# Performance work log

Measured on AMD Instinct MI355X. Metric: run time of the kernel, lower is better.

The kernel has to match this reference:

```python
import jax, jax.numpy as jnp
import numpy as np

DIM = 1024


def setup_inputs() -> dict:
    key = jax.random.key(0)
    ks = jax.random.split(key, 10)
    B, S, D = 4, 2048, DIM
    std = 1.0 / np.sqrt(D)  # torch Linear default uniform bound
    return {
        "query": jax.random.normal(ks[0], (B, S, D), jnp.float32),
        "key": jax.random.normal(ks[1], (B, S, D), jnp.float32),
        "value": jax.random.normal(ks[2], (B, S, D), jnp.float32),
        "context": jnp.zeros((D,), jnp.float32),
        "Wq": jax.random.uniform(ks[3], (D, D), jnp.float32, -std, std),
        "bq": jax.random.uniform(ks[4], (D,), jnp.float32, -std, std),
        "Wk": jax.random.uniform(ks[5], (D, D), jnp.float32, -std, std),
        "bk": jax.random.uniform(ks[6], (D,), jnp.float32, -std, std),
        "Wv": jax.random.uniform(ks[7], (D, D), jnp.float32, -std, std),
        "bv": jax.random.uniform(ks[8], (D,), jnp.float32, -std, std),
    }


def reference(query, key, value, context, Wq, bq, Wk, bk, Wv, bv):
    scale = query.shape[-1] ** -0.5
    # torch Linear: x @ W.T + b
    q = (query + context) @ Wq.T + bq          # [B,S,D]
    k = (key + context) @ Wk.T + bk            # [B,S,D]
    v = value @ Wv.T + bv                      # [B,S,D]
    scores = jnp.einsum("bqd,bkd->bqk", q, k) * scale  # [B,S,S]
    weights = jax.nn.softmax(scores, axis=-1)
    return jnp.einsum("bqk,bkd->bqd", weights, v)
```

## Files before the change

### kernel.cpp

```cpp
#include <hip/hip_runtime.h>

typedef __attribute__((ext_vector_type(8))) short bf16x8;
typedef __attribute__((ext_vector_type(4))) float floatx4;

constexpr int BATCH = 4;
constexpr int SEQ   = 2048;
constexpr int DIMN  = 1024;
constexpr int M1    = BATCH * SEQ;

__device__ __forceinline__ short f2bf(float f) {
    union { float f; unsigned u; } x; x.f = f;
    unsigned r = x.u + 0x7fffu + ((x.u >> 16) & 1u);
    return (short)(r >> 16);
}
__device__ __forceinline__ float bf2f(short s) {
    union { unsigned u; float f; } x; x.u = ((unsigned)(unsigned short)s) << 16;
    return x.f;
}

__device__ __forceinline__ void async16(const void* g, void* l) {
    __builtin_amdgcn_global_load_lds(
        (const __attribute__((address_space(1))) unsigned int*)g,
        (__attribute__((address_space(3))) unsigned int*)l, 16, 0, 0);
}

#define WAITVM(N) asm volatile("s_waitcnt vmcnt(" #N ")" ::: "memory")
#define MEMFENCE  asm volatile("" ::: "memory")
#define BAR()     __builtin_amdgcn_s_barrier()
#define PRIO(x)   __builtin_amdgcn_s_setprio(x)

template<bool OUT_BF16>
__device__ __forceinline__ void gemm128(
    const short* __restrict__ Ab, int lda,
    const short* __restrict__ Bb, int ldb,
    void* __restrict__ Cb, int ldc,
    const float* __restrict__ bias, int K, float scale,
    int m0, int n0)
{
    constexpr int ABY  = 16384;
    constexpr int BUFB = ABY + 32768;
    __shared__ alignas(16) char smem[3 * BUFB];
    char* lds = smem;

    const int t    = threadIdx.x;
    const int lane = t & 63;
    const int wave = t >> 6;
    const int wr   = wave >> 2;
    const int wc   = wave & 3;
    const int lr   = lane & 15;
    const int lq   = lane >> 4;

    const int srow  = t >> 3;
    const int scol  = (((t & 7) * 16) ^ ((srow & 7) << 4)) >> 1;
    const short* pa0 = Ab + (size_t)(m0 + srow) * lda + scol;
    const short* pb0 = Bb + (size_t)(n0 + srow) * ldb + scol;
    const size_t rsa = (size_t)64 * lda;
    const size_t rsb = (size_t)64 * ldb;
    const int ldst = t * 16;

    const int roA = (wr * 64 + lr) * 128;
    const int roB = ABY + (wc * 64 + lr) * 128;
    const int cs  = (lane & 7) << 4;
    const int cp0 = (lq << 4) ^ cs;
    const int cp1 = (64 | (lq << 4)) ^ cs;

    floatx4 acc[4][4];
    #pragma unroll
    for (int m = 0; m < 4; ++m)
        #pragma unroll
        for (int n = 0; n < 4; ++n) acc[m][n] = (floatx4)(0.f);

    auto stA = [&](int d, int kt) { const short* p = pa0 + kt * 64;
        async16(p,       lds + d +        ldst);
        async16(p + rsa, lds + d + 8192 + ldst); };
    auto stB01 = [&](int d, int kt) { const short* p = pb0 + kt * 64;
        async16(p,       lds + d + ABY +        ldst);
        async16(p + rsb, lds + d + ABY + 8192 + ldst); };
    auto stB23 = [&](int d, int kt) { const short* p = pb0 + kt * 64;
        async16(p + 2 * rsb, lds + d + ABY + 16384 + ldst);
        async16(p + 3 * rsb, lds + d + ABY + 24576 + ldst); };

    const int NT = K >> 6;

    stA(0, 0); stB01(0, 0); stB23(0, 0);
    if (NT > 1) { stA(BUFB, 1); stB01(BUFB, 1); stB23(BUFB, 1); WAITVM(6); }
    else        { WAITVM(0); }
    BAR(); MEMFENCE;

    int cb = 0;
    for (int tt = 0; tt < NT; ++tt) {
        const char* rb = lds + cb;
        int sb = cb + 2 * BUFB; if (sb >= 3 * BUFB) sb -= 3 * BUFB;
        bf16x8 a[4], b[4];

        #pragma unroll
        for (int m = 0; m < 4; ++m) a[m] = *(const bf16x8*)(rb + roA + m * 2048 + cp0);
        #pragma unroll
        for (int n = 0; n < 4; ++n) b[n] = *(const bf16x8*)(rb + roB + n * 2048 + cp0);
        if (tt + 2 < NT) { stA(sb, tt + 2); stB01(sb, tt + 2); }
        BAR(); MEMFENCE;
        PRIO(1);
        #pragma unroll
        for (int m = 0; m < 4; ++m)
            #pragma unroll
            for (int n = 0; n < 4; ++n)
                acc[m][n] = __builtin_amdgcn_mfma_f32_16x16x32_bf16(a[m], b[n], acc[m][n], 0, 0, 0);
        PRIO(0); MEMFENCE;
        BAR(); MEMFENCE;

        #pragma unroll
        for (int m = 0; m < 4; ++m) a[m] = *(const bf16x8*)(rb + roA + m * 2048 + cp1);
        #pragma unroll
        for (int n = 0; n < 4; ++n) b[n] = *(const bf16x8*)(rb + roB + n * 2048 + cp1);
        if (tt + 2 < NT) stB23(sb, tt + 2);
        BAR(); MEMFENCE;
        PRIO(1);
        #pragma unroll
        for (int m = 0; m < 4; ++m)
            #pragma unroll
            for (int n = 0; n < 4; ++n)
                acc[m][n] = __builtin_amdgcn_mfma_f32_16x16x32_bf16(a[m], b[n], acc[m][n], 0, 0, 0);
        PRIO(0); MEMFENCE;
        if (tt + 1 < NT) {
            if (tt + 2 < NT) { WAITVM(6); } else { WAITVM(0); }
        }
        BAR(); MEMFENCE;
        cb += BUFB; if (cb >= 3 * BUFB) cb = 0;
    }

    #pragma unroll
    for (int n = 0; n < 4; ++n) {
        const int gn = n0 + wc * 64 + n * 16 + lr;
        const float bv = bias ? bias[gn] : 0.f;
        #pragma unroll
        for (int m = 0; m < 4; ++m) {
            #pragma unroll
            for (int r = 0; r < 4; ++r) {
                const int gm = m0 + wr * 64 + m * 16 + lq * 4 + r;
                const float v = acc[m][n][r] * scale + bv;
                if (OUT_BF16) ((short*)Cb)[(size_t)gm * ldc + gn] = f2bf(v);
                else          ((float*)Cb)[(size_t)gm * ldc + gn] = v;
            }
        }
    }
}

__global__ __launch_bounds__(512, 2)
void proj_qkv(const short* __restrict__ xq, const short* __restrict__ xk,
              const short* __restrict__ xv,
              const short* __restrict__ Wq_, const short* __restrict__ Wk_,
              const short* __restrict__ Wv_,
              const float* __restrict__ bq_, const float* __restrict__ bk_,
              const float* __restrict__ bv_,
              short* __restrict__ q, short* __restrict__ k, short* __restrict__ vp)
{
    const int b   = blockIdx.x;
    const int xcd = b & 7;
    const int i   = b >> 3;
    const int z   = i >> 5;
    const int r   = i & 31;
    const int mm  = r >> 2;
    const int nn  = r & 3;
    const short* X = (z == 0) ? xq : (z == 1) ? xk : xv;
    const short* W = (z == 0) ? Wq_ : (z == 1) ? Wk_ : Wv_;
    const float* bb = (z == 0) ? bq_ : (z == 1) ? bk_ : bv_;
    short* O = (z == 0) ? q : (z == 1) ? k : vp;
    gemm128<true>(X, DIMN, W, DIMN, (void*)O, DIMN, bb, DIMN, 1.f,
                  (xcd * 8 + mm) * 128, nn * 256);
}

__global__ __launch_bounds__(512, 2)
void gemm_scores(const short* __restrict__ q, const short* __restrict__ k,
                 short* __restrict__ S, float scale)
{
    const int b   = blockIdx.x;
    const int xcd = b & 7;
    const int i   = b >> 3;
    const int bz  = xcd >> 1;
    const int mh  = xcd & 1;
    const int mm  = i >> 3;
    const int nn  = i & 7;
    gemm128<true>(q + (size_t)bz * SEQ * DIMN, DIMN,
                  k + (size_t)bz * SEQ * DIMN, DIMN,
                  (void*)(S + (size_t)bz * SEQ * SEQ), SEQ,
                  nullptr, DIMN, scale,
                  (mh * 8 + mm) * 128, nn * 256);
}

__global__ __launch_bounds__(512, 2)
void gemm_pv(const short* __restrict__ P, const short* __restrict__ vt,
             float* __restrict__ O)
{
    const int b   = blockIdx.x;
    const int xcd = b & 7;
    const int i   = b >> 3;
    const int bz  = xcd >> 1;
    const int mh  = xcd & 1;
    const int mm  = i >> 2;
    const int nn  = i & 3;
    gemm128<false>(P  + (size_t)bz * SEQ * SEQ,  SEQ,
                   vt + (size_t)bz * DIMN * SEQ, SEQ,
                   (void*)(O + (size_t)bz * SEQ * DIMN), DIMN,
                   nullptr, SEQ, 1.f,
                   (mh * 8 + mm) * 128, nn * 256);
}

__global__ __launch_bounds__(256)
void cvt6(const float* __restrict__ w0, short* __restrict__ ow0,
          const float* __restrict__ w1, short* __restrict__ ow1,
          const float* __restrict__ w2, short* __restrict__ ow2,
          const float* __restrict__ x0, short* __restrict__ ox0,
          const float* __restrict__ x1, short* __restrict__ ox1,
          const float* __restrict__ x2, short* __restrict__ ox2,
          int n8w, int n8x)
{
    const int z = blockIdx.z;
    const float* in; short* out; int n8;
    switch (z) {
        case 0: in = w0; out = ow0; n8 = n8w; break;
        case 1: in = w1; out = ow1; n8 = n8w; break;
        case 2: in = w2; out = ow2; n8 = n8w; break;
        case 3: in = x0; out = ox0; n8 = n8x; break;
        case 4: in = x1; out = ox1; n8 = n8x; break;
        default: in = x2; out = ox2; n8 = n8x; break;
    }
    const int i = blockIdx.x * 256 + threadIdx.x;
    if (i >= n8) return;
    const float4 a0 = ((const float4*)in)[(size_t)i * 2];
    const float4 a1 = ((const float4*)in)[(size_t)i * 2 + 1];
    const float v[8] = {a0.x, a0.y, a0.z, a0.w, a1.x, a1.y, a1.z, a1.w};
    bf16x8 o;
    #pragma unroll
    for (int j = 0; j < 8; ++j) o[j] = f2bf(v[j]);
    *(bf16x8*)(out + (size_t)i * 8) = o;
}

__global__ __launch_bounds__(256)
void bias3(const float* __restrict__ Wq, const float* __restrict__ Wk,
           const float* __restrict__ Wv,
           const float* __restrict__ bq, const float* __restrict__ bk,
           const float* __restrict__ bv,
           const float* __restrict__ ctx,
           float* __restrict__ oq, float* __restrict__ ok, float* __restrict__ ov)
{
    const int z = blockIdx.y;
    const float* W = (z == 0) ? Wq : (z == 1) ? Wk : Wv;
    const float* b = (z == 0) ? bq : (z == 1) ? bk : bv;
    float*       o = (z == 0) ? oq : (z == 1) ? ok : ov;
    const int n    = blockIdx.x * 4 + (threadIdx.x >> 6);
    const int lane = threadIdx.x & 63;
    float s = 0.f;
    if (z < 2) {
        const float* row = W + (size_t)n * DIMN;
        for (int k = lane * 4; k < DIMN; k += 256) {
            const float4 x = *(const float4*)(row + k);
            const float4 c = *(const float4*)(ctx + k);
            s += x.x * c.x + x.y * c.y + x.z * c.z + x.w * c.w;
        }
        #pragma unroll
        for (int off = 32; off > 0; off >>= 1) s += __shfl_xor(s, off);
    }
    if (lane == 0) o[n] = b[n] + s;
}

__global__ __launch_bounds__(256)
void transpose_v(const short* __restrict__ in, short* __restrict__ out)
{
    __shared__ short t[64][68];
    const int b  = blockIdx.z;
    const int d0 = blockIdx.x * 64;
    const int s0 = blockIdx.y * 64;
    const int r  = threadIdx.x >> 3;
    const int c  = (threadIdx.x & 7) * 8;
    #pragma unroll
    for (int h = 0; h < 2; ++h) {
        const int s = r + h * 32;
        bf16x8 v = *(const bf16x8*)(in + ((size_t)b * SEQ + s0 + s) * DIMN + d0 + c);
        #pragma unroll
        for (int j = 0; j < 8; ++j) t[c + j][s] = v[j];
    }
    __syncthreads();
    #pragma unroll
    for (int h = 0; h < 2; ++h) {
        const int d = r + h * 32;
        bf16x8 v;
        #pragma unroll
        for (int j = 0; j < 8; ++j) v[j] = t[d][c + j];
        *(bf16x8*)(out + ((size_t)b * DIMN + d0 + d) * SEQ + s0 + c) = v;
    }
}

__global__ __launch_bounds__(256)
void softmax_kernel(short* __restrict__ P)
{
    const int bid = blockIdx.x;
    const int xcd = bid & 7;
    const int i   = bid >> 3;
    const int row = (xcd >> 1) * SEQ + (xcd & 1) * 1024 + i;
    short* p = P + (size_t)row * SEQ;
    const int t    = threadIdx.x;
    const int lane = t & 63;
    const int wave = t >> 6;
    __shared__ float red[8];

    bf16x8 raw = *(const bf16x8*)(p + t * 8);
    float v[8];
    float mx = -1e30f;
    #pragma unroll
    for (int j = 0; j < 8; ++j) { v[j] = bf2f(raw[j]); mx = fmaxf(mx, v[j]); }
    #pragma unroll
    for (int off = 32; off > 0; off >>= 1) mx = fmaxf(mx, __shfl_xor(mx, off));
    if (lane == 0) red[wave] = mx;
    __syncthreads();
    mx = fmaxf(fmaxf(red[0], red[1]), fmaxf(red[2], red[3]));

    float e[8], s = 0.f;
    #pragma unroll
    for (int j = 0; j < 8; ++j) { e[j] = __expf(v[j] - mx); s += e[j]; }
    #pragma unroll
    for (int off = 32; off > 0; off >>= 1) s += __shfl_xor(s, off);
    if (lane == 0) red[4 + wave] = s;
    __syncthreads();
    s = red[4] + red[5] + red[6] + red[7];
    const float inv = 1.f / s;

    bf16x8 o;
    #pragma unroll
    for (int j = 0; j < 8; ++j) o[j] = f2bf(e[j] * inv);
    *(bf16x8*)(p + t * 8) = o;
}

extern "C" void kernel_launch(void* const* d_in, const int* in_sizes, int n_in,
                              void* d_out, int out_size, void* d_ws, size_t ws_size,
                              hipStream_t stream)
{
    const float* query = (const float*)d_in[0];
    const float* key_  = (const float*)d_in[1];
    const float* value = (const float*)d_in[2];
    const float* ctx   = (const float*)d_in[3];
    const float* Wq    = (const float*)d_in[4];
    const float* bq    = (const float*)d_in[5];
    const float* Wk    = (const float*)d_in[6];
    const float* bk    = (const float*)d_in[7];
    const float* Wv    = (const float*)d_in[8];
    const float* bv    = (const float*)d_in[9];

    char* ws = (char*)d_ws;
    char* od = (char*)d_out;
    const size_t MB = 1ull << 20;
    short* xq   = (short*)(ws);
    short* xk   = (short*)(ws + 16 * MB);
    short* q_b  = (short*)(ws + 32 * MB);
    short* k_b  = (short*)(ws + 48 * MB);
    short* Wq_b = (short*)(ws + 64 * MB);
    short* Wk_b = (short*)(ws + 66 * MB);
    short* Wv_b = (short*)(ws + 68 * MB);
    float* bq_e = (float*)(ws + 70 * MB);
    float* bk_e = (float*)(ws + 70 * MB + 4096);
    float* bv_e = (float*)(ws + 70 * MB + 8192);
    short* S_b  = (short*)(ws);
    short* v_t  = (short*)(ws + 64 * MB);
    short* xv   = (short*)(od);
    short* vp   = (short*)(od + 16 * MB);

    dim3 blk(256);
    dim3 blk512(512);
    const int W8 = DIMN * DIMN / 8;
    const int X8 = M1 * DIMN / 8;

    cvt6<<<dim3(X8 / 256, 1, 6), blk, 0, stream>>>(Wq, Wq_b, Wk, Wk_b, Wv, Wv_b,
                                                   query, xq, key_, xk, value, xv,
                                                   W8, X8);
    bias3<<<dim3(DIMN / 4, 3), blk, 0, stream>>>(Wq, Wk, Wv, bq, bk, bv, ctx,
                                                 bq_e, bk_e, bv_e);

    proj_qkv<<<dim3(768), blk512, 0, stream>>>(xq, xk, xv, Wq_b, Wk_b, Wv_b,
                                               bq_e, bk_e, bv_e, q_b, k_b, vp);
    transpose_v<<<dim3(DIMN / 64, SEQ / 64, BATCH), blk, 0, stream>>>(vp, v_t);

    const float scale = 1.0f / 32.0f;
    gemm_scores<<<dim3(512), blk512, 0, stream>>>(q_b, k_b, S_b, scale);

    softmax_kernel<<<dim3(M1), blk, 0, stream>>>(S_b);

    gemm_pv<<<dim3(256), blk512, 0, stream>>>(S_b, v_t, (float*)d_out);
}
```

Baseline: 302.4 us.

## Use 32x32 MFMA, compute V projection transposed directly, fuse bias into convert

The shared GEMM now uses 32x32x16 bf16 MFMA tiles instead of 16x16x32, which lowers the LDS read count per FLOP. The V projection is computed as Wv·Xv^T with a per-row bias, so it writes V transposed directly and the separate transpose kernel is gone. The bias-fold kernel is merged into the conversion kernel as an extra grid slice, and workspace buffers are moved around. Together these remove two launches and a round trip of V through memory, in exchange for a different accumulator layout and strided epilogue stores.

```diff
diff --git a/kernel.cpp b/kernel.cpp
--- a/kernel.cpp
+++ b/kernel.cpp
@@ -2,12 +2,17 @@
 
 typedef __attribute__((ext_vector_type(8))) short bf16x8;
 typedef __attribute__((ext_vector_type(4))) float floatx4;
+typedef __attribute__((ext_vector_type(16))) float floatx16;
 
 constexpr int BATCH = 4;
 constexpr int SEQ   = 2048;
 constexpr int DIMN  = 1024;
 constexpr int M1    = BATCH * SEQ;
 
+constexpr int G_ABY  = 16384;
+constexpr int G_BUFB = G_ABY + 32768;
+constexpr int G_LDSZ = 3 * G_BUFB;
+
 __device__ __forceinline__ short f2bf(float f) {
     union { float f; unsigned u; } x; x.f = f;
     unsigned r = x.u + 0x7fffu + ((x.u >> 16) & 1u);
@@ -29,26 +34,23 @@
 #define BAR()     __builtin_amdgcn_s_barrier()
 #define PRIO(x)   __builtin_amdgcn_s_setprio(x)
 
-template<bool OUT_BF16>
+template<bool OUT_BF16, int BMODE>
 __device__ __forceinline__ void gemm128(
+    char* __restrict__ lds,
     const short* __restrict__ Ab, int lda,
     const short* __restrict__ Bb, int ldb,
     void* __restrict__ Cb, int ldc,
     const float* __restrict__ bias, int K, float scale,
     int m0, int n0)
 {
-    constexpr int ABY  = 16384;
-    constexpr int BUFB = ABY + 32768;
-    __shared__ alignas(16) char smem[3 * BUFB];
-    char* lds = smem;
+    constexpr int ABY  = G_ABY;
+    constexpr int BUFB = G_BUFB;
 
     const int t    = threadIdx.x;
     const int lane = t & 63;
     const int wave = t >> 6;
     const int wr   = wave >> 2;
     const int wc   = wave & 3;
-    const int lr   = lane & 15;
-    const int lq   = lane >> 4;
 
     const int srow  = t >> 3;
     const int scol  = (((t & 7) * 16) ^ ((srow & 7) << 4)) >> 1;
@@ -58,17 +60,22 @@
     const size_t rsb = (size_t)64 * ldb;
     const int ldst = t * 16;
 
-    const int roA = (wr * 64 + lr) * 128;
-    const int roB = ABY + (wc * 64 + lr) * 128;
-    const int cs  = (lane & 7) << 4;
-    const int cp0 = (lq << 4) ^ cs;
-    const int cp1 = (64 | (lq << 4)) ^ cs;
-
-    floatx4 acc[4][4];
-    #pragma unroll
-    for (int m = 0; m < 4; ++m)
-        #pragma unroll
-        for (int n = 0; n < 4; ++n) acc[m][n] = (floatx4)(0.f);
+    const int l31   = lane & 31;
+    const int swz   = (lane & 7) << 4;
+    const int khalf = (lane >> 5) << 4;
+    int colp[4];
+    #pragma unroll
+    for (int ks = 0; ks < 4; ++ks) colp[ks] = (ks * 32 + khalf) ^ swz;
+    const int roA = (wr * 64 + l31) * 128;
+    const int roB = ABY + (wc * 64 + l31) * 128;
+
+    floatx16 acc[2][2];
+    #pragma unroll
+    for (int mi = 0; mi < 2; ++mi)
+        #pragma unroll
+        for (int ni = 0; ni < 2; ++ni)
+            #pragma unroll
+            for (int r = 0; r < 16; ++r) acc[mi][ni][r] = 0.f;
 
     auto stA = [&](int d, int kt) { const short* p = pa0 + kt * 64;
         async16(p,       lds + d +        ldst);
@@ -91,35 +98,53 @@
     for (int tt = 0; tt < NT; ++tt) {
         const char* rb = lds + cb;
         int sb = cb + 2 * BUFB; if (sb >= 3 * BUFB) sb -= 3 * BUFB;
-        bf16x8 a[4], b[4];
-
-        #pragma unroll
-        for (int m = 0; m < 4; ++m) a[m] = *(const bf16x8*)(rb + roA + m * 2048 + cp0);
-        #pragma unroll
-        for (int n = 0; n < 4; ++n) b[n] = *(const bf16x8*)(rb + roB + n * 2048 + cp0);
+        bf16x8 a[2][2], b[2][2];
+
+        #pragma unroll
+        for (int mi = 0; mi < 2; ++mi)
+            #pragma unroll
+            for (int ks = 0; ks < 2; ++ks)
+                a[mi][ks] = *(const bf16x8*)(rb + roA + mi * 4096 + colp[ks]);
+        #pragma unroll
+        for (int ni = 0; ni < 2; ++ni)
+            #pragma unroll
+            for (int ks = 0; ks < 2; ++ks)
+                b[ni][ks] = *(const bf16x8*)(rb + roB + ni * 4096 + colp[ks]);
         if (tt + 2 < NT) { stA(sb, tt + 2); stB01(sb, tt + 2); }
         BAR(); MEMFENCE;
         PRIO(1);
         #pragma unroll
-        for (int m = 0; m < 4; ++m)
-            #pragma unroll
-            for (int n = 0; n < 4; ++n)
-                acc[m][n] = __builtin_amdgcn_mfma_f32_16x16x32_bf16(a[m], b[n], acc[m][n], 0, 0, 0);
+        for (int ks = 0; ks < 2; ++ks)
+            #pragma unroll
+            for (int mi = 0; mi < 2; ++mi)
+                #pragma unroll
+                for (int ni = 0; ni < 2; ++ni)
+                    acc[mi][ni] = __builtin_amdgcn_mfma_f32_32x32x16_bf16(
+                        a[mi][ks], b[ni][ks], acc[mi][ni], 0, 0, 0);
         PRIO(0); MEMFENCE;
         BAR(); MEMFENCE;
 
         #pragma unroll
-        for (int m = 0; m < 4; ++m) a[m] = *(const bf16x8*)(rb + roA + m * 2048 + cp1);
-        #pragma unroll
-        for (int n = 0; n < 4; ++n) b[n] = *(const bf16x8*)(rb + roB + n * 2048 + cp1);
+        for (int mi = 0; mi < 2; ++mi)
+            #pragma unroll
+            for (int ks = 0; ks < 2; ++ks)
+                a[mi][ks] = *(const bf16x8*)(rb + roA + mi * 4096 + colp[ks + 2]);
+        #pragma unroll
+        for (int ni = 0; ni < 2; ++ni)
+            #pragma unroll
+            for (int ks = 0; ks < 2; ++ks)
+                b[ni][ks] = *(const bf16x8*)(rb + roB + ni * 4096 + colp[ks + 2]);
         if (tt + 2 < NT) stB23(sb, tt + 2);
         BAR(); MEMFENCE;
         PRIO(1);
         #pragma unroll
-        for (int m = 0; m < 4; ++m)
-            #pragma unroll
-            for (int n = 0; n < 4; ++n)
-                acc[m][n] = __builtin_amdgcn_mfma_f32_16x16x32_bf16(a[m], b[n], acc[m][n], 0, 0, 0);
+        for (int ks = 0; ks < 2; ++ks)
+            #pragma unroll
+            for (int mi = 0; mi < 2; ++mi)
+                #pragma unroll
+                for (int ni = 0; ni < 2; ++ni)
+                    acc[mi][ni] = __builtin_amdgcn_mfma_f32_32x32x16_bf16(
+                        a[mi][ks], b[ni][ks], acc[mi][ni], 0, 0, 0);
         PRIO(0); MEMFENCE;
         if (tt + 1 < NT) {
             if (tt + 2 < NT) { WAITVM(6); } else { WAITVM(0); }
@@ -128,16 +153,22 @@
         cb += BUFB; if (cb >= 3 * BUFB) cb = 0;
     }
 
-    #pragma unroll
-    for (int n = 0; n < 4; ++n) {
-        const int gn = n0 + wc * 64 + n * 16 + lr;
-        const float bv = bias ? bias[gn] : 0.f;
-        #pragma unroll
-        for (int m = 0; m < 4; ++m) {
-            #pragma unroll
-            for (int r = 0; r < 4; ++r) {
-                const int gm = m0 + wr * 64 + m * 16 + lq * 4 + r;
-                const float v = acc[m][n][r] * scale + bv;
+    const int rhi = (lane >> 5) * 4;
+    #pragma unroll
+    for (int mi = 0; mi < 2; ++mi) {
+        #pragma unroll
+        for (int ni = 0; ni < 2; ++ni) {
+            const int gm0 = m0 + wr * 64 + mi * 32;
+            const int gn  = n0 + wc * 64 + ni * 32 + l31;
+            float cbv = 0.f;
+            if (BMODE == 1) cbv = bias[gn];
+            #pragma unroll
+            for (int r = 0; r < 16; ++r) {
+                const int row = (r & 3) + 8 * (r >> 2) + rhi;
+                const int gm  = gm0 + row;
+                float v = acc[mi][ni][r] * scale;
+                if (BMODE == 1) v += cbv;
+                if (BMODE == 2) v += bias[gm];
                 if (OUT_BF16) ((short*)Cb)[(size_t)gm * ldc + gn] = f2bf(v);
                 else          ((float*)Cb)[(size_t)gm * ldc + gn] = v;
             }
@@ -152,27 +183,40 @@
               const short* __restrict__ Wv_,
               const float* __restrict__ bq_, const float* __restrict__ bk_,
               const float* __restrict__ bv_,
-              short* __restrict__ q, short* __restrict__ k, short* __restrict__ vp)
-{
+              short* __restrict__ q, short* __restrict__ k, short* __restrict__ vt)
+{
+    __shared__ alignas(16) char smem[G_LDSZ];
     const int b   = blockIdx.x;
     const int xcd = b & 7;
     const int i   = b >> 3;
-    const int z   = i >> 5;
-    const int r   = i & 31;
-    const int mm  = r >> 2;
-    const int nn  = r & 3;
-    const short* X = (z == 0) ? xq : (z == 1) ? xk : xv;
-    const short* W = (z == 0) ? Wq_ : (z == 1) ? Wk_ : Wv_;
-    const float* bb = (z == 0) ? bq_ : (z == 1) ? bk_ : bv_;
-    short* O = (z == 0) ? q : (z == 1) ? k : vp;
-    gemm128<true>(X, DIMN, W, DIMN, (void*)O, DIMN, bb, DIMN, 1.f,
-                  (xcd * 8 + mm) * 128, nn * 256);
+    if (i < 64) {
+        const int z   = i >> 5;
+        const int r   = i & 31;
+        const int mm  = r >> 2;
+        const int nn  = r & 3;
+        const short* X = (z == 0) ? xq : xk;
+        const short* W = (z == 0) ? Wq_ : Wk_;
+        const float* bb = (z == 0) ? bq_ : bk_;
+        short* O = (z == 0) ? q : k;
+        gemm128<true, 1>(smem, X, DIMN, W, DIMN, (void*)O, DIMN, bb, DIMN, 1.f,
+                         (xcd * 8 + mm) * 128, nn * 256);
+    } else {
+        const int r  = i - 64;
+        const int bz = r >> 3;
+        const int nn = r & 7;
+        gemm128<true, 2>(smem, Wv_, DIMN,
+                         xv + (size_t)bz * SEQ * DIMN, DIMN,
+                         (void*)(vt + (size_t)bz * DIMN * SEQ), SEQ,
+                         bv_, DIMN, 1.f,
+                         xcd * 128, nn * 256);
+    }
 }
 
 __global__ __launch_bounds__(512, 2)
 void gemm_scores(const short* __restrict__ q, const short* __restrict__ k,
                  short* __restrict__ S, float scale)
 {
+    __shared__ alignas(16) char smem[G_LDSZ];
     const int b   = blockIdx.x;
     const int xcd = b & 7;
     const int i   = b >> 3;
@@ -180,17 +224,18 @@
     const int mh  = xcd & 1;
     const int mm  = i >> 3;
     const int nn  = i & 7;
-    gemm128<true>(q + (size_t)bz * SEQ * DIMN, DIMN,
-                  k + (size_t)bz * SEQ * DIMN, DIMN,
-                  (void*)(S + (size_t)bz * SEQ * SEQ), SEQ,
-                  nullptr, DIMN, scale,
-                  (mh * 8 + mm) * 128, nn * 256);
+    gemm128<true, 0>(smem, q + (size_t)bz * SEQ * DIMN, DIMN,
+                     k + (size_t)bz * SEQ * DIMN, DIMN,
+                     (void*)(S + (size_t)bz * SEQ * SEQ), SEQ,
+                     nullptr, DIMN, scale,
+                     (mh * 8 + mm) * 128, nn * 256);
 }
 
 __global__ __launch_bounds__(512, 2)
 void gemm_pv(const short* __restrict__ P, const short* __restrict__ vt,
              float* __restrict__ O)
 {
+    __shared__ alignas(16) char smem[G_LDSZ];
     const int b   = blockIdx.x;
     const int xcd = b & 7;
     const int i   = b >> 3;
@@ -198,23 +243,49 @@
     const int mh  = xcd & 1;
     const int mm  = i >> 2;
     const int nn  = i & 3;
-    gemm128<false>(P  + (size_t)bz * SEQ * SEQ,  SEQ,
-                   vt + (size_t)bz * DIMN * SEQ, SEQ,
-                   (void*)(O + (size_t)bz * SEQ * DIMN), DIMN,
-                   nullptr, SEQ, 1.f,
-                   (mh * 8 + mm) * 128, nn * 256);
+    gemm128<false, 0>(smem, P  + (size_t)bz * SEQ * SEQ,  SEQ,
+                      vt + (size_t)bz * DIMN * SEQ, SEQ,
+                      (void*)(O + (size_t)bz * SEQ * DIMN), DIMN,
+                      nullptr, SEQ, 1.f,
+                      (mh * 8 + mm) * 128, nn * 256);
 }
 
 __global__ __launch_bounds__(256)
-void cvt6(const float* __restrict__ w0, short* __restrict__ ow0,
+void cvt7(const float* __restrict__ w0, short* __restrict__ ow0,
           const float* __restrict__ w1, short* __restrict__ ow1,
           const float* __restrict__ w2, short* __restrict__ ow2,
           const float* __restrict__ x0, short* __restrict__ ox0,
           const float* __restrict__ x1, short* __restrict__ ox1,
           const float* __restrict__ x2, short* __restrict__ ox2,
+          const float* __restrict__ bq, const float* __restrict__ bk,
+          const float* __restrict__ bv, const float* __restrict__ ctx,
+          float* __restrict__ oq, float* __restrict__ ok, float* __restrict__ ov,
           int n8w, int n8x)
 {
     const int z = blockIdx.z;
+    if (z == 6) {
+        const int bx = blockIdx.x;
+        if (bx >= 768) return;
+        const int z2 = bx >> 8;
+        const float* W = (z2 == 0) ? w0 : (z2 == 1) ? w1 : w2;
+        const float* bb = (z2 == 0) ? bq : (z2 == 1) ? bk : bv;
+        float*       o  = (z2 == 0) ? oq : (z2 == 1) ? ok : ov;
+        const int n    = (bx & 255) * 4 + (threadIdx.x >> 6);
+        const int lane = threadIdx.x & 63;
+        float s = 0.f;
+        if (z2 < 2) {
+            const float* row = W + (size_t)n * DIMN;
+            for (int kk = lane * 4; kk < DIMN; kk += 256) {
+                const float4 x = *(const float4*)(row + kk);
+                const float4 c = *(const float4*)(ctx + kk);
+                s += x.x * c.x + x.y * c.y + x.z * c.z + x.w * c.w;
+            }
+            #pragma unroll
+            for (int off = 32; off > 0; off >>= 1) s += __shfl_xor(s, off);
+        }
+        if (lane == 0) o[n] = bb[n] + s;
+        return;
+    }
     const float* in; short* out; int n8;
     switch (z) {
         case 0: in = w0; out = ow0; n8 = n8w; break;
@@ -236,61 +307,6 @@
 }
 
 __global__ __launch_bounds__(256)
-void bias3(const float* __restrict__ Wq, const float* __restrict__ Wk,
-           const float* __restrict__ Wv,
-           const float* __restrict__ bq, const float* __restrict__ bk,
-           const float* __restrict__ bv,
-           const float* __restrict__ ctx,
-           float* __restrict__ oq, float* __restrict__ ok, float* __restrict__ ov)
-{
-    const int z = blockIdx.y;
-    const float* W = (z == 0) ? Wq : (z == 1) ? Wk : Wv;
-    const float* b = (z == 0) ? bq : (z == 1) ? bk : bv;
-    float*       o = (z == 0) ? oq : (z == 1) ? ok : ov;
-    const int n    = blockIdx.x * 4 + (threadIdx.x >> 6);
-    const int lane = threadIdx.x & 63;
-    float s = 0.f;
-    if (z < 2) {
-        const float* row = W + (size_t)n * DIMN;
-        for (int k = lane * 4; k < DIMN; k += 256) {
-            const float4 x = *(const float4*)(row + k);
-            const float4 c = *(const float4*)(ctx + k);
-            s += x.x * c.x + x.y * c.y + x.z * c.z + x.w * c.w;
-        }
-        #pragma unroll
-        for (int off = 32; off > 0; off >>= 1) s += __shfl_xor(s, off);
-    }
-    if (lane == 0) o[n] = b[n] + s;
-}
-
-__global__ __launch_bounds__(256)
-void transpose_v(const short* __restrict__ in, short* __restrict__ out)
-{
-    __shared__ short t[64][68];
-    const int b  = blockIdx.z;
-    const int d0 = blockIdx.x * 64;
-    const int s0 = blockIdx.y * 64;
-    const int r  = threadIdx.x >> 3;
-    const int c  = (threadIdx.x & 7) * 8;
-    #pragma unroll
-    for (int h = 0; h < 2; ++h) {
-        const int s = r + h * 32;
-        bf16x8 v = *(const bf16x8*)(in + ((size_t)b * SEQ + s0 + s) * DIMN + d0 + c);
-        #pragma unroll
-        for (int j = 0; j < 8; ++j) t[c + j][s] = v[j];
-    }
-    __syncthreads();
-    #pragma unroll
-    for (int h = 0; h < 2; ++h) {
-        const int d = r + h * 32;
-        bf16x8 v;
-        #pragma unroll
-        for (int j = 0; j < 8; ++j) v[j] = t[d][c + j];
-        *(bf16x8*)(out + ((size_t)b * DIMN + d0 + d) * SEQ + s0 + c) = v;
-    }
-}
-
-__global__ __launch_bounds__(256)
 void softmax_kernel(short* __restrict__ P)
 {
     const int bid = blockIdx.x;
@@ -352,31 +368,29 @@
     short* xk   = (short*)(ws + 16 * MB);
     short* q_b  = (short*)(ws + 32 * MB);
     short* k_b  = (short*)(ws + 48 * MB);
-    short* Wq_b = (short*)(ws + 64 * MB);
-    short* Wk_b = (short*)(ws + 66 * MB);
-    short* Wv_b = (short*)(ws + 68 * MB);
-    float* bq_e = (float*)(ws + 70 * MB);
-    float* bk_e = (float*)(ws + 70 * MB + 4096);
-    float* bv_e = (float*)(ws + 70 * MB + 8192);
+    short* v_t  = (short*)(ws + 64 * MB);
     short* S_b  = (short*)(ws);
-    short* v_t  = (short*)(ws + 64 * MB);
     short* xv   = (short*)(od);
-    short* vp   = (short*)(od + 16 * MB);
+    short* Wq_b = (short*)(od + 16 * MB);
+    short* Wk_b = (short*)(od + 18 * MB);
+    short* Wv_b = (short*)(od + 20 * MB);
+    float* bq_e = (float*)(od + 22 * MB);
+    float* bk_e = (float*)(od + 22 * MB + 4096);
+    float* bv_e = (float*)(od + 22 * MB + 8192);
 
     dim3 blk(256);
     dim3 blk512(512);
     const int W8 = DIMN * DIMN / 8;
     const int X8 = M1 * DIMN / 8;
 
-    cvt6<<<dim3(X8 / 256, 1, 6), blk, 0, stream>>>(Wq, Wq_b, Wk, Wk_b, Wv, Wv_b,
-                                                   query, xq, key_, xk, value, xv,
-                                                   W8, X8);
-    bias3<<<dim3(DIMN / 4, 3), blk, 0, stream>>>(Wq, Wk, Wv, bq, bk, bv, ctx,
-                                                 bq_e, bk_e, bv_e);
+    cvt7<<<dim3(X8 / 256, 1, 7), blk, 0, stream>>>(
+        Wq, Wq_b, Wk, Wk_b, Wv, Wv_b,
+        query, xq, key_, xk, value, xv,
+        bq, bk, bv, ctx, bq_e, bk_e, bv_e,
+        W8, X8);
 
     proj_qkv<<<dim3(768), blk512, 0, stream>>>(xq, xk, xv, Wq_b, Wk_b, Wv_b,
-                                               bq_e, bk_e, bv_e, q_b, k_b, vp);
-    transpose_v<<<dim3(DIMN / 64, SEQ / 64, BATCH), blk, 0, stream>>>(vp, v_t);
+                                               bq_e, bk_e, bv_e, q_b, k_b, v_t);
 
     const float scale = 1.0f / 32.0f;
     gemm_scores<<<dim3(512), blk512, 0, stream>>>(q_b, k_b, S_b, scale);
```

Result: no change. 308.0 us (+1.9%).
